# Kernel optimization log

Hardware: AMD Instinct MI355X
Metric: run time of the kernel (lower is better)

## Reference

```python
import jax, jax.numpy as jnp
import numpy as np

N_NODES = 50000
N_EDGES = 800000
D_IN, D_HID, D_OUT = 256, 128, 64
NEG_SLOPE = 0.2  # PyG GATConv default


def gat_conv(x, W, a_src, a_dst, b, src, dst, n):
    """Single-head PyG-style GATConv with self-loops already in (src, dst)."""
    h = x @ W                                  # [N, d_out]
    # per-edge attention logits: LeakyReLU(a_src . h_src + a_dst . h_dst)
    e = jax.nn.leaky_relu((h @ a_src)[src] + (h @ a_dst)[dst], NEG_SLOPE)  # [E]
    # segment softmax over incoming edges of each dst node (stable)
    e = e - jax.ops.segment_max(e, dst, num_segments=n)[dst]
    p = jnp.exp(e)
    p = p / jax.ops.segment_sum(p, dst, num_segments=n)[dst]
    # weighted scatter-add of source messages
    out = jax.ops.segment_sum(p[:, None] * h[src], dst, num_segments=n)
    return out + b


def setup_inputs() -> dict:
    key = jax.random.key(0)
    ks = jax.random.split(key, 10)
    x = jax.random.normal(ks[0], (N_NODES, D_IN), dtype=jnp.float32)
    edge_index = jax.random.randint(ks[1], (2, N_EDGES), 0, N_NODES, dtype=jnp.int32)
    s1 = 1.0 / np.sqrt(D_IN)
    s2 = 1.0 / np.sqrt(D_HID)
    W1 = jax.random.normal(ks[2], (D_IN, D_HID), dtype=jnp.float32) * s1
    a_src1 = jax.random.normal(ks[3], (D_HID,), dtype=jnp.float32) * s2
    a_dst1 = jax.random.normal(ks[4], (D_HID,), dtype=jnp.float32) * s2
    b1 = jnp.zeros((D_HID,), dtype=jnp.float32)
    W2 = jax.random.normal(ks[5], (D_HID, D_OUT), dtype=jnp.float32) * s2
    a_src2 = jax.random.normal(ks[6], (D_OUT,), dtype=jnp.float32) * (1.0 / np.sqrt(D_OUT))
    a_dst2 = jax.random.normal(ks[7], (D_OUT,), dtype=jnp.float32) * (1.0 / np.sqrt(D_OUT))
    b2 = jnp.zeros((D_OUT,), dtype=jnp.float32)
    return {"x": x, "edge_index": edge_index, "W1": W1, "a_src1": a_src1,
            "a_dst1": a_dst1, "b1": b1, "W2": W2, "a_src2": a_src2,
            "a_dst2": a_dst2, "b2": b2}


def reference(x, edge_index, W1, a_src1, a_dst1, b1, W2, a_src2, a_dst2, b2):
    n = x.shape[0]
    loops = jnp.arange(n, dtype=edge_index.dtype)
    src = jnp.concatenate([edge_index[0], loops])  # add_self_loops=True (PyG default)
    dst = jnp.concatenate([edge_index[1], loops])
    h = gat_conv(x, W1, a_src1, a_dst1, b1, src, dst, n)
    h = jax.nn.relu(h)
    return gat_conv(h, W2, a_src2, a_dst2, b2, src, dst, n)
```

## Files before the change

kernel.cpp:

```cpp
#include <hip/hip_runtime.h>
#include <stdint.h>

#define DIN 256
#define DHID 128
#define DOUTD 64
#define NBLK 128

typedef __attribute__((ext_vector_type(8))) short bf16x8;
typedef __attribute__((ext_vector_type(4))) float f32x4;

__device__ __forceinline__ uint32_t pack_bf16x2(float x, float y) {
    uint32_t ux = __builtin_bit_cast(uint32_t, x);
    uint32_t uy = __builtin_bit_cast(uint32_t, y);
    ux += 0x7fffu + ((ux >> 16) & 1u);
    uy += 0x7fffu + ((uy >> 16) & 1u);
    return (ux >> 16) | (uy & 0xffff0000u);
}
__device__ __forceinline__ uint16_t to_bf16(float x) {
    uint32_t u = __builtin_bit_cast(uint32_t, x);
    u += 0x7fffu + ((u >> 16) & 1u);
    return (uint16_t)(u >> 16);
}
__device__ __forceinline__ float bflo(uint32_t v) { return __builtin_bit_cast(float, v << 16); }
__device__ __forceinline__ float bfhi(uint32_t v) { return __builtin_bit_cast(float, v & 0xffff0000u); }

template<int K, int N>
__device__ __forceinline__ void prepack_body(
    const float* __restrict__ W, uint16_t* __restrict__ Bp, int t)
{
    constexpr int CB = N / 16;
    if (t >= (K / 32) * CB * 64) return;
    const int lane = t & 63, fi = t >> 6;
    const int c = fi % CB, kb = fi / CB;
    const int j  = 16 * c + (lane & 15);
    const int k0 = kb * 32 + (lane >> 4) * 8;
    uint32_t o[4];
    #pragma unroll
    for (int i = 0; i < 4; ++i) {
        float lo = W[(size_t)(k0 + 2 * i)     * N + j];
        float hi = W[(size_t)(k0 + 2 * i + 1) * N + j];
        o[i] = pack_bf16x2(lo, hi);
    }
    *reinterpret_cast<uint4*>(&Bp[(size_t)t * 8]) = make_uint4(o[0], o[1], o[2], o[3]);
}

__global__ __launch_bounds__(256) void prepack_both_kernel(
    const float* __restrict__ W1, uint16_t* __restrict__ Bp1,
    const float* __restrict__ W2, uint16_t* __restrict__ Bp2)
{
    if (blockIdx.x < 16)
        prepack_body<DIN, DHID>(W1, Bp1, blockIdx.x * 256 + threadIdx.x);
    else
        prepack_body<DHID, DOUTD>(W2, Bp2, (blockIdx.x - 16) * 256 + threadIdx.x);
}

template<int K, int N, bool AF32>
__global__ __launch_bounds__(256) void mfma_gemm(
    const void* __restrict__ A, const uint16_t* __restrict__ Bp,
    uint16_t* __restrict__ Cout, const float* __restrict__ a_s,
    const float* __restrict__ a_d, float* __restrict__ asrc,
    float* __restrict__ adst, int M)
{
    constexpr int KB = K / 32, CB = N / 16;
    __shared__ __align__(16) uint16_t As[64 * K];

    const int tid = threadIdx.x;
    const int row0 = blockIdx.x * 64;

    if (AF32) {
        constexpr int NIT = 64 * K / 4 / 256;
        #pragma unroll
        for (int i = 0; i < NIT; ++i) {
            int u = tid + i * 256;
            int row = u / (K / 4);
            int k4  = (u % (K / 4)) * 4;
            float4 v = make_float4(0.f, 0.f, 0.f, 0.f);
            if (row0 + row < M)
                v = *reinterpret_cast<const float4*>((const float*)A + (size_t)(row0 + row) * K + k4);
            uint32_t byte = (uint32_t)row * (K * 2) + k4 * 2;
            byte ^= (row & 7) << 4;
            *reinterpret_cast<uint2*>((char*)As + byte) =
                make_uint2(pack_bf16x2(v.x, v.y), pack_bf16x2(v.z, v.w));
        }
    } else {
        constexpr int NIT = 64 * K / 8 / 256;
        #pragma unroll
        for (int i = 0; i < NIT; ++i) {
            int u = tid + i * 256;
            int row = u / (K / 8);
            int k8  = (u % (K / 8)) * 8;
            uint4 v = make_uint4(0u, 0u, 0u, 0u);
            if (row0 + row < M)
                v = *reinterpret_cast<const uint4*>((const uint16_t*)A + (size_t)(row0 + row) * K + k8);
            uint32_t byte = (uint32_t)row * (K * 2) + k8 * 2;
            byte ^= (row & 7) << 4;
            *reinterpret_cast<uint4*>((char*)As + byte) = v;
        }
    }
    __syncthreads();

    const int w = tid >> 6, l = tid & 63;
    const int rA = w * 16 + (l & 15);

    f32x4 acc[CB] = {};
    const char* blane = (const char*)Bp + l * 16;

    #pragma unroll
    for (int kb = 0; kb < KB; ++kb) {
        uint32_t abyte = (uint32_t)rA * (K * 2) + (kb * 32 + (l >> 4) * 8) * 2;
        abyte ^= (rA & 7) << 4;
        bf16x8 a = *reinterpret_cast<const bf16x8*>((const char*)As + abyte);
        #pragma unroll
        for (int c = 0; c < CB; ++c) {
            bf16x8 b = *reinterpret_cast<const bf16x8*>(blane + (size_t)(kb * CB + c) * 1024);
            acc[c] = __builtin_amdgcn_mfma_f32_16x16x32_bf16(a, b, acc[c], 0, 0, 0);
        }
    }

    const int rb = w * 16 + (l >> 4) * 4;
    const int colb = l & 15;

    #pragma unroll
    for (int c = 0; c < CB; ++c) {
        #pragma unroll
        for (int r = 0; r < 4; ++r) {
            int grow = row0 + rb + r;
            if (grow < M)
                Cout[(size_t)grow * N + c * 16 + colb] = to_bf16(acc[c][r]);
        }
    }

    float ps[4] = {}, pd[4] = {};
    #pragma unroll
    for (int c = 0; c < CB; ++c) {
        float asv = a_s[c * 16 + colb];
        float adv = a_d[c * 16 + colb];
        #pragma unroll
        for (int r = 0; r < 4; ++r) {
            ps[r] += acc[c][r] * asv;
            pd[r] += acc[c][r] * adv;
        }
    }
    #pragma unroll
    for (int mask = 1; mask < 16; mask <<= 1) {
        #pragma unroll
        for (int r = 0; r < 4; ++r) {
            ps[r] += __shfl_xor(ps[r], mask);
            pd[r] += __shfl_xor(pd[r], mask);
        }
    }
    if (colb == 0) {
        #pragma unroll
        for (int r = 0; r < 4; ++r) {
            int grow = row0 + rb + r;
            if (grow < M) { asrc[grow] = ps[r]; adst[grow] = pd[r]; }
        }
    }
}

__global__ __launch_bounds__(256) void histB_kernel(
    const int* __restrict__ ei, int E, int n, int nbuck, int chunk,
    int* __restrict__ F)
{
    __shared__ int h[512];
    for (int i = threadIdx.x; i < nbuck; i += 256) h[i] = 0;
    __syncthreads();
    const int blk = blockIdx.x;
    const int ET = E + n;
    const int e0 = blk * chunk, e1 = min(e0 + chunk, ET);
    for (int e = e0 + threadIdx.x; e < e1; e += 256) {
        int d = (e < E) ? ei[E + e] : (e - E);
        atomicAdd(&h[d >> 7], 1);
    }
    __syncthreads();
    for (int i = threadIdx.x; i < nbuck; i += 256)
        F[i * NBLK + blk] = h[i];
}

__global__ void scan1_kernel(const int* __restrict__ deg, int n,
                             int* __restrict__ S, int* __restrict__ part)
{
    __shared__ int sm[256];
    int i = blockIdx.x * 256 + threadIdx.x;
    int v = (i < n) ? deg[i] : 0;
    sm[threadIdx.x] = v;
    __syncthreads();
    for (int off = 1; off < 256; off <<= 1) {
        int t = (threadIdx.x >= off) ? sm[threadIdx.x - off] : 0;
        __syncthreads();
        sm[threadIdx.x] += t;
        __syncthreads();
    }
    if (i < n) S[i] = sm[threadIdx.x];
    if (threadIdx.x == 255) part[blockIdx.x] = sm[255];
}

__global__ void scan2_kernel(int* __restrict__ part, int nb)
{
    __shared__ int sm[256];
    int v = (threadIdx.x < nb) ? part[threadIdx.x] : 0;
    sm[threadIdx.x] = v;
    __syncthreads();
    for (int off = 1; off < 256; off <<= 1) {
        int t = (threadIdx.x >= off) ? sm[threadIdx.x - off] : 0;
        __syncthreads();
        sm[threadIdx.x] += t;
        __syncthreads();
    }
    if (threadIdx.x < nb)
        part[threadIdx.x] = (threadIdx.x == 0) ? 0 : sm[threadIdx.x - 1];
}

__global__ void scan3_kernel(const int* __restrict__ S, const int* __restrict__ part,
                             int n, int* __restrict__ P)
{
    int i = blockIdx.x * 256 + threadIdx.x;
    if (i < n) P[i + 1] = S[i] + part[i / 256];
    if (i == 0) P[0] = 0;
}

__global__ __launch_bounds__(256) void scatterB_kernel(
    const int* __restrict__ ei, int E, int n, int nbuck, int chunk,
    const int* __restrict__ P, uint32_t* __restrict__ bucketed)
{
    __shared__ int cur[512];
    const int blk = blockIdx.x;
    for (int i = threadIdx.x; i < nbuck; i += 256) cur[i] = P[i * NBLK + blk];
    __syncthreads();
    const int ET = E + n;
    const int e0 = blk * chunk, e1 = min(e0 + chunk, ET);
    for (int e = e0 + threadIdx.x; e < e1; e += 256) {
        int s, d;
        if (e < E) { s = ei[e]; d = ei[E + e]; }
        else       { s = e - E; d = s; }
        int pos = atomicAdd(&cur[d >> 7], 1);
        bucketed[pos] = ((uint32_t)d << 16) | (uint32_t)s;
    }
}

__global__ __launch_bounds__(256) void csrF_kernel(
    const uint32_t* __restrict__ bucketed, const int* __restrict__ P,
    int n, int* __restrict__ offs, int* __restrict__ csr)
{
    __shared__ int hist[128];
    __shared__ int scn[128];
    __shared__ int cur[128];
    const int b = blockIdx.x;
    const int tid = threadIdx.x;
    const int beg = P[b * NBLK];
    const int end = P[(b + 1) * NBLK];

    if (tid < 128) hist[tid] = 0;
    __syncthreads();
    for (int i = beg + tid; i < end; i += 256)
        atomicAdd(&hist[(bucketed[i] >> 16) & 127], 1);
    __syncthreads();
    if (tid < 128) scn[tid] = hist[tid];
    __syncthreads();
    #pragma unroll
    for (int off = 1; off < 128; off <<= 1) {
        int v = (tid < 128 && tid >= off) ? scn[tid - off] : 0;
        __syncthreads();
        if (tid < 128) scn[tid] += v;
        __syncthreads();
    }
    if (tid < 128) {
        int excl = (tid == 0) ? 0 : scn[tid - 1];
        cur[tid] = beg + excl;
        int node = b * 128 + tid;
        if (node <= n) offs[node] = beg + excl;
    }
    __syncthreads();
    for (int i = beg + tid; i < end; i += 256) {
        uint32_t pk = bucketed[i];
        int pos = atomicAdd(&cur[(pk >> 16) & 127], 1);
        csr[pos] = (int)(pk & 0xFFFFu);
    }
}

template<int D, bool RELU, bool OUTB16>
__global__ __launch_bounds__(256) void agg_kernel(
    const uint32_t* __restrict__ Hb, const float* __restrict__ asrc,
    const float* __restrict__ adst, const int* __restrict__ offs,
    const int* __restrict__ csr_src, const float* __restrict__ bias,
    void* __restrict__ out, int n)
{
    constexpr int C16 = D / 8;
    constexpr int EPI = 64 / C16;
    const int wid = threadIdx.x >> 6, lane = threadIdx.x & 63;
    const int node = blockIdx.x * 4 + wid;
    if (node >= n) return;

    const int beg = offs[node];
    const int deg = offs[node + 1] - beg;
    const float ad = adst[node];
    const int seg = lane / C16;
    const int chk = lane & (C16 - 1);

    float acc[8] = {};
    float ssum = 0.f;

    for (int base = 0; base < deg; base += 64) {
        const int lim = min(64, deg - base);
        float wt = 0.f; int st = 0;
        if (lane < lim) {
            st = csr_src[beg + base + lane];
            float t = asrc[st] + ad;
            t = (t > 0.f) ? t : 0.2f * t;
            wt = __expf(t);
        }
        ssum += wt;
        const int iters = (lim + EPI - 1) / EPI;
        #pragma unroll 2
        for (int it = 0; it < iters; ++it) {
            int e = it * EPI + seg;
            float we = __shfl(wt, e);
            int   se = __shfl(st, e);
            uint4 v = *(reinterpret_cast<const uint4*>(Hb) + (size_t)se * (D / 8) + chk);
            acc[0] += we * bflo(v.x); acc[1] += we * bfhi(v.x);
            acc[2] += we * bflo(v.y); acc[3] += we * bfhi(v.y);
            acc[4] += we * bflo(v.z); acc[5] += we * bfhi(v.z);
            acc[6] += we * bflo(v.w); acc[7] += we * bfhi(v.w);
        }
    }

    #pragma unroll
    for (int mask = C16; mask < 64; mask <<= 1)
        #pragma unroll
        for (int j = 0; j < 8; ++j)
            acc[j] += __shfl_xor(acc[j], mask);
    #pragma unroll
    for (int off = 32; off; off >>= 1) ssum += __shfl_xor(ssum, off);
    const float inv = 1.f / ssum;

    if (seg == 0) {
        const int col0 = chk * 8;
        float r[8];
        #pragma unroll
        for (int j = 0; j < 8; ++j) {
            r[j] = acc[j] * inv + bias[col0 + j];
            if (RELU) r[j] = fmaxf(r[j], 0.f);
        }
        if (OUTB16) {
            uint4 o = make_uint4(pack_bf16x2(r[0], r[1]), pack_bf16x2(r[2], r[3]),
                                 pack_bf16x2(r[4], r[5]), pack_bf16x2(r[6], r[7]));
            *(reinterpret_cast<uint4*>(out) + (size_t)node * (D / 8) + chk) = o;
        } else {
            float* op = (float*)out + (size_t)node * D + col0;
            *reinterpret_cast<float4*>(op)     = make_float4(r[0], r[1], r[2], r[3]);
            *reinterpret_cast<float4*>(op + 4) = make_float4(r[4], r[5], r[6], r[7]);
        }
    }
}

extern "C" void kernel_launch(void* const* d_in, const int* in_sizes, int n_in,
                              void* d_out, int out_size, void* d_ws, size_t ws_size,
                              hipStream_t stream)
{
    const float* x   = (const float*)d_in[0];
    const int*   ei  = (const int*)  d_in[1];
    const float* W1  = (const float*)d_in[2];
    const float* as1 = (const float*)d_in[3];
    const float* ad1 = (const float*)d_in[4];
    const float* b1  = (const float*)d_in[5];
    const float* W2  = (const float*)d_in[6];
    const float* as2 = (const float*)d_in[7];
    const float* ad2 = (const float*)d_in[8];
    const float* b2  = (const float*)d_in[9];
    float* out = (float*)d_out;

    const int n  = in_sizes[0] / DIN;
    const int E  = in_sizes[1] / 2;
    const int ET = E + n;

    const int nbuck  = (n + 127) >> 7;
    const int nbtot  = nbuck * NBLK;
    const int chunk  = (ET + NBLK - 1) / NBLK;

    char* ws = (char*)d_ws;
    size_t off = 0;
    auto alloc = [&](size_t bytes) -> void* {
        off = (off + 255) & ~(size_t)255;
        void* p = ws + off;
        off += bytes;
        return p;
    };
    uint16_t* Hb   = (uint16_t*)alloc((size_t)n * DHID * 2);
    uint16_t* O1b  = (uint16_t*)alloc((size_t)n * DHID * 2);
    uint16_t* H2b  = (uint16_t*)alloc((size_t)n * DOUTD * 2);
    float* asrc    = (float*)alloc((size_t)n * 4);
    float* adst    = (float*)alloc((size_t)n * 4);
    uint16_t* Bp1  = (uint16_t*)alloc((size_t)DIN * DHID * 2);
    uint16_t* Bp2  = (uint16_t*)alloc((size_t)DHID * DOUTD * 2);
    int* F     = (int*)alloc((size_t)nbtot * 4);
    int* S     = (int*)alloc((size_t)nbtot * 4);
    int* part  = (int*)alloc(256 * 4);
    int* P     = (int*)alloc((size_t)(nbtot + 1) * 4);
    int* offs  = (int*)alloc((size_t)(n + 1) * 4);
    uint32_t* bucketed = (uint32_t*)alloc((size_t)ET * 4);
    int* csr   = (int*)alloc((size_t)ET * 4);

    const int nbs = (nbtot + 255) / 256;
    const int nw  = (n + 3) / 4;
    const int ng  = (n + 63) / 64;

    prepack_both_kernel<<<20, 256, 0, stream>>>(W1, Bp1, W2, Bp2);

    histB_kernel<<<NBLK, 256, 0, stream>>>(ei, E, n, nbuck, chunk, F);
    scan1_kernel<<<nbs, 256, 0, stream>>>(F, nbtot, S, part);
    scan2_kernel<<<1, 256, 0, stream>>>(part, nbs);
    scan3_kernel<<<nbs, 256, 0, stream>>>(S, part, nbtot, P);
    scatterB_kernel<<<NBLK, 256, 0, stream>>>(ei, E, n, nbuck, chunk, P, bucketed);
    csrF_kernel<<<nbuck, 256, 0, stream>>>(bucketed, P, n, offs, csr);

    mfma_gemm<DIN, DHID, true><<<ng, 256, 0, stream>>>(x, Bp1, Hb, as1, ad1, asrc, adst, n);
    agg_kernel<DHID, true, true><<<nw, 256, 0, stream>>>(
        (const uint32_t*)Hb, asrc, adst, offs, csr, b1, O1b, n);

    mfma_gemm<DHID, DOUTD, false><<<ng, 256, 0, stream>>>(O1b, Bp2, H2b, as2, ad2, asrc, adst, n);
    agg_kernel<DOUTD, false, false><<<nw, 256, 0, stream>>>(
        (const uint32_t*)H2b, asrc, adst, offs, csr, b2, out, n);
}
```

Baseline: 228.6 us.

## Replace multi-kernel scan CSR build with fixed-capacity buckets and atomic reservation

Merges the histogram and scatter passes into one kernel. Each block now reserves space in a fixed-capacity region per 128-node bucket (BCAP slots) with a global atomicAdd, which removes the three prefix-scan kernels and the separate histogram launch. The CSR pass then reads per-bucket counts and writes an explicit per-node degree array used by aggregation. The cost is padded workspace and an unchecked assumption that no bucket holds more than 4096 edges; this holds for uniformly random graphs but could overflow on skewed inputs. Edge order within a bucket also becomes nondeterministic.

```diff
diff --git a/kernel.cpp b/kernel.cpp
--- a/kernel.cpp
+++ b/kernel.cpp
@@ -5,6 +5,7 @@
 #define DHID 128
 #define DOUTD 64
 #define NBLK 128
+#define BCAP 4096
 
 typedef __attribute__((ext_vector_type(8))) short bf16x8;
 typedef __attribute__((ext_vector_type(4))) float f32x4;
@@ -158,11 +159,12 @@
     }
 }
 
-__global__ __launch_bounds__(256) void histB_kernel(
+__global__ __launch_bounds__(256) void histscatter_kernel(
     const int* __restrict__ ei, int E, int n, int nbuck, int chunk,
-    int* __restrict__ F)
+    int* __restrict__ cntG, uint32_t* __restrict__ bucketed)
 {
     __shared__ int h[512];
+    __shared__ int curL[512];
     for (int i = threadIdx.x; i < nbuck; i += 256) h[i] = 0;
     __syncthreads();
     const int blk = blockIdx.x;
@@ -173,82 +175,33 @@
         atomicAdd(&h[d >> 7], 1);
     }
     __syncthreads();
-    for (int i = threadIdx.x; i < nbuck; i += 256)
-        F[i * NBLK + blk] = h[i];
-}
-
-__global__ void scan1_kernel(const int* __restrict__ deg, int n,
-                             int* __restrict__ S, int* __restrict__ part)
-{
-    __shared__ int sm[256];
-    int i = blockIdx.x * 256 + threadIdx.x;
-    int v = (i < n) ? deg[i] : 0;
-    sm[threadIdx.x] = v;
-    __syncthreads();
-    for (int off = 1; off < 256; off <<= 1) {
-        int t = (threadIdx.x >= off) ? sm[threadIdx.x - off] : 0;
-        __syncthreads();
-        sm[threadIdx.x] += t;
-        __syncthreads();
-    }
-    if (i < n) S[i] = sm[threadIdx.x];
-    if (threadIdx.x == 255) part[blockIdx.x] = sm[255];
-}
-
-__global__ void scan2_kernel(int* __restrict__ part, int nb)
-{
-    __shared__ int sm[256];
-    int v = (threadIdx.x < nb) ? part[threadIdx.x] : 0;
-    sm[threadIdx.x] = v;
-    __syncthreads();
-    for (int off = 1; off < 256; off <<= 1) {
-        int t = (threadIdx.x >= off) ? sm[threadIdx.x - off] : 0;
-        __syncthreads();
-        sm[threadIdx.x] += t;
-        __syncthreads();
-    }
-    if (threadIdx.x < nb)
-        part[threadIdx.x] = (threadIdx.x == 0) ? 0 : sm[threadIdx.x - 1];
-}
-
-__global__ void scan3_kernel(const int* __restrict__ S, const int* __restrict__ part,
-                             int n, int* __restrict__ P)
-{
-    int i = blockIdx.x * 256 + threadIdx.x;
-    if (i < n) P[i + 1] = S[i] + part[i / 256];
-    if (i == 0) P[0] = 0;
-}
-
-__global__ __launch_bounds__(256) void scatterB_kernel(
-    const int* __restrict__ ei, int E, int n, int nbuck, int chunk,
-    const int* __restrict__ P, uint32_t* __restrict__ bucketed)
-{
-    __shared__ int cur[512];
-    const int blk = blockIdx.x;
-    for (int i = threadIdx.x; i < nbuck; i += 256) cur[i] = P[i * NBLK + blk];
-    __syncthreads();
-    const int ET = E + n;
-    const int e0 = blk * chunk, e1 = min(e0 + chunk, ET);
+    for (int i = threadIdx.x; i < nbuck; i += 256) {
+        int c = h[i];
+        int base = i * BCAP;
+        if (c) base += atomicAdd(&cntG[i], c);
+        curL[i] = base;
+    }
+    __syncthreads();
     for (int e = e0 + threadIdx.x; e < e1; e += 256) {
         int s, d;
         if (e < E) { s = ei[e]; d = ei[E + e]; }
         else       { s = e - E; d = s; }
-        int pos = atomicAdd(&cur[d >> 7], 1);
+        int pos = atomicAdd(&curL[d >> 7], 1);
         bucketed[pos] = ((uint32_t)d << 16) | (uint32_t)s;
     }
 }
 
 __global__ __launch_bounds__(256) void csrF_kernel(
-    const uint32_t* __restrict__ bucketed, const int* __restrict__ P,
-    int n, int* __restrict__ offs, int* __restrict__ csr)
+    const uint32_t* __restrict__ bucketed, const int* __restrict__ cntG,
+    int n, int* __restrict__ offs, int* __restrict__ degs, int* __restrict__ csr)
 {
     __shared__ int hist[128];
     __shared__ int scn[128];
     __shared__ int cur[128];
     const int b = blockIdx.x;
     const int tid = threadIdx.x;
-    const int beg = P[b * NBLK];
-    const int end = P[(b + 1) * NBLK];
+    const int beg = b * BCAP;
+    const int end = beg + cntG[b];
 
     if (tid < 128) hist[tid] = 0;
     __syncthreads();
@@ -268,7 +221,7 @@
         int excl = (tid == 0) ? 0 : scn[tid - 1];
         cur[tid] = beg + excl;
         int node = b * 128 + tid;
-        if (node <= n) offs[node] = beg + excl;
+        if (node < n) { offs[node] = beg + excl; degs[node] = hist[tid]; }
     }
     __syncthreads();
     for (int i = beg + tid; i < end; i += 256) {
@@ -282,8 +235,8 @@
 __global__ __launch_bounds__(256) void agg_kernel(
     const uint32_t* __restrict__ Hb, const float* __restrict__ asrc,
     const float* __restrict__ adst, const int* __restrict__ offs,
-    const int* __restrict__ csr_src, const float* __restrict__ bias,
-    void* __restrict__ out, int n)
+    const int* __restrict__ degs, const int* __restrict__ csr_src,
+    const float* __restrict__ bias, void* __restrict__ out, int n)
 {
     constexpr int C16 = D / 8;
     constexpr int EPI = 64 / C16;
@@ -292,7 +245,7 @@
     if (node >= n) return;
 
     const int beg = offs[node];
-    const int deg = offs[node + 1] - beg;
+    const int deg = degs[node];
     const float ad = adst[node];
     const int seg = lane / C16;
     const int chk = lane & (C16 - 1);
@@ -374,7 +327,6 @@
     const int ET = E + n;
 
     const int nbuck  = (n + 127) >> 7;
-    const int nbtot  = nbuck * NBLK;
     const int chunk  = (ET + NBLK - 1) / NBLK;
 
     char* ws = (char*)d_ws;
@@ -392,32 +344,26 @@
     float* adst    = (float*)alloc((size_t)n * 4);
     uint16_t* Bp1  = (uint16_t*)alloc((size_t)DIN * DHID * 2);
     uint16_t* Bp2  = (uint16_t*)alloc((size_t)DHID * DOUTD * 2);
-    int* F     = (int*)alloc((size_t)nbtot * 4);
-    int* S     = (int*)alloc((size_t)nbtot * 4);
-    int* part  = (int*)alloc(256 * 4);
-    int* P     = (int*)alloc((size_t)(nbtot + 1) * 4);
-    int* offs  = (int*)alloc((size_t)(n + 1) * 4);
-    uint32_t* bucketed = (uint32_t*)alloc((size_t)ET * 4);
-    int* csr   = (int*)alloc((size_t)ET * 4);
-
-    const int nbs = (nbtot + 255) / 256;
-    const int nw  = (n + 3) / 4;
-    const int ng  = (n + 63) / 64;
-
+    int* cntG  = (int*)alloc((size_t)nbuck * 4);
+    int* offs  = (int*)alloc((size_t)n * 4);
+    int* degs  = (int*)alloc((size_t)n * 4);
+    uint32_t* bucketed = (uint32_t*)alloc((size_t)nbuck * BCAP * 4);
+    int* csr   = (int*)alloc((size_t)nbuck * BCAP * 4);
+
+    const int nw = (n + 3) / 4;
+    const int ng = (n + 63) / 64;
+
+    hipMemsetAsync(cntG, 0, (size_t)nbuck * 4, stream);
     prepack_both_kernel<<<20, 256, 0, stream>>>(W1, Bp1, W2, Bp2);
 
-    histB_kernel<<<NBLK, 256, 0, stream>>>(ei, E, n, nbuck, chunk, F);
-    scan1_kernel<<<nbs, 256, 0, stream>>>(F, nbtot, S, part);
-    scan2_kernel<<<1, 256, 0, stream>>>(part, nbs);
-    scan3_kernel<<<nbs, 256, 0, stream>>>(S, part, nbtot, P);
-    scatterB_kernel<<<NBLK, 256, 0, stream>>>(ei, E, n, nbuck, chunk, P, bucketed);
-    csrF_kernel<<<nbuck, 256, 0, stream>>>(bucketed, P, n, offs, csr);
+    histscatter_kernel<<<NBLK, 256, 0, stream>>>(ei, E, n, nbuck, chunk, cntG, bucketed);
+    csrF_kernel<<<nbuck, 256, 0, stream>>>(bucketed, cntG, n, offs, degs, csr);
 
     mfma_gemm<DIN, DHID, true><<<ng, 256, 0, stream>>>(x, Bp1, Hb, as1, ad1, asrc, adst, n);
     agg_kernel<DHID, true, true><<<nw, 256, 0, stream>>>(
-        (const uint32_t*)Hb, asrc, adst, offs, csr, b1, O1b, n);
+        (const uint32_t*)Hb, asrc, adst, offs, degs, csr, b1, O1b, n);
 
     mfma_gemm<DHID, DOUTD, false><<<ng, 256, 0, stream>>>(O1b, Bp2, H2b, as2, ad2, asrc, adst, n);
     agg_kernel<DOUTD, false, false><<<nw, 256, 0, stream>>>(
-        (const uint32_t*)H2b, asrc, adst, offs, csr, b2, out, n);
-}
+        (const uint32_t*)H2b, asrc, adst, offs, degs, csr, b2, out, n);
+}
```

Result: no change. 229.3 us (+0.3%).
